# Kernel optimization log

Hardware: AMD Instinct MI355X
Metric: run time of the kernel (lower is better)

## Reference

```python
import jax, jax.numpy as jnp
import numpy as np

B, C, H, W = 8, 128, 64, 64

def setup_inputs() -> dict:
    key = jax.random.key(0)
    ks = jax.random.split(key, 8)
    s = 1.0 / np.sqrt(C)
    return {
        "x": jax.random.normal(ks[0], (B, C, H, W), dtype=jnp.float32),
        "dw_q": jax.random.normal(ks[1], (C,), dtype=jnp.float32) * s,
        "pw_q": jax.random.normal(ks[2], (C, C), dtype=jnp.float32) * s,
        "dw_k": jax.random.normal(ks[3], (C,), dtype=jnp.float32) * s,
        "pw_k": jax.random.normal(ks[4], (C, C), dtype=jnp.float32) * s,
        "dw_v": jax.random.normal(ks[5], (C,), dtype=jnp.float32) * s,
        "pw_v": jax.random.normal(ks[6], (C, C), dtype=jnp.float32) * s,
        "gamma": jnp.zeros((1,), dtype=jnp.float32) + 0.5,
    }

def _proj(x, dw, pw):
    # depthwise 1x1 (groups=C, no bias) == per-channel scale; then pointwise 1x1 conv (C_out=C)
    xs = x * dw[None, :, None, None]
    return jnp.einsum('oc,bchw->bohw', pw, xs)

def reference(x, dw_q, pw_q, dw_k, pw_k, dw_v, pw_v, gamma):
    b, c, h, w = x.shape
    n = h * w
    q = _proj(x, dw_q, pw_q).reshape(b, c, n)   # B,C,N
    k = _proj(x, dw_k, pw_k).reshape(b, c, n)
    v = _proj(x, dw_v, pw_v).reshape(b, c, n)
    # energy[b,n,m] = sum_c q[b,c,n] k[b,c,m]  (no scaling, as in source)
    energy = jnp.einsum('bcn,bcm->bnm', q, k)
    attn = jax.nn.softmax(energy, axis=-1)      # B,N,N
    # out[b,c,n] = sum_m v[b,c,m] attn[b,n,m]
    out = jnp.einsum('bcm,bnm->bcn', v, attn).reshape(b, c, h, w)
    return gamma[0] * out + x
```

## Files before the change

### kernel.cpp

```cpp
#include <hip/hip_runtime.h>
#include <hip/hip_bf16.h>


typedef __bf16 v8bf __attribute__((ext_vector_type(8)));
typedef float  v4f  __attribute__((ext_vector_type(4)));
typedef unsigned long long u64;

#define B_ 8
#define C_ 128
#define N_ 4096

#define SWZ(R, COLS) ((R) * 160 + (((((COLS) >> 3) ^ (((R) >> 2) & 15))) << 3) + ((COLS) & 7))

static __device__ __forceinline__ unsigned short f2bf_rne(float f) {
    union { float f; unsigned u; } v; v.f = f;
    return (unsigned short)((v.u + 0x7fffu + ((v.u >> 16) & 1u)) >> 16);
}

static __device__ __forceinline__ u64 bf8pack(uint4 s) {
    float f[8];
    #pragma unroll
    for (int j = 0; j < 8; ++j) {
        unsigned hs = (j & 1) ? ((&s.x)[j >> 1] >> 16) : ((&s.x)[j >> 1] & 0xffffu);
        union { unsigned u; float f; } t; t.u = hs << 16; f[j] = t.f;
    }
    int lo = __builtin_amdgcn_cvt_pk_fp8_f32(f[0], f[1], 0, false);
    lo     = __builtin_amdgcn_cvt_pk_fp8_f32(f[2], f[3], lo, true);
    int hi = __builtin_amdgcn_cvt_pk_fp8_f32(f[4], f[5], 0, false);
    hi     = __builtin_amdgcn_cvt_pk_fp8_f32(f[6], f[7], hi, true);
    return (u64)(unsigned)lo | ((u64)(unsigned)hi << 32);
}

__global__ __launch_bounds__(256, 2) void proj_kernel(
    const float* __restrict__ x,
    const float* __restrict__ dw_q, const float* __restrict__ pw_q,
    const float* __restrict__ dw_k, const float* __restrict__ pw_k,
    const float* __restrict__ dw_v, const float* __restrict__ pw_v,
    unsigned char* __restrict__ qf8, unsigned char* __restrict__ kt8,
    unsigned char* __restrict__ vt8)
{
    __shared__ unsigned short xT[128 * 160];
    __shared__ unsigned short Ws[128 * 160];

    const int bid = blockIdx.x;
    const int bb  = bid & 7;
    const int t   = (bid >> 3) & 31;
    const int pp  = bid >> 8;
    const int n0  = t * 128;
    const int tid = threadIdx.x;
    const int w    = tid >> 6;
    const int lane = tid & 63;
    const int quad = lane >> 4;
    const int l16  = lane & 15;

    #pragma unroll
    for (int k = 0; k < 16; ++k) {
        const int idx = tid + k * 256;
        const int c  = idx >> 5;
        const int nq = idx & 31;
        float4 f = *(const float4*)(x + ((size_t)(bb * C_ + c)) * N_ + n0 + nq * 4);
        xT[SWZ(nq * 4 + 0, c)] = f2bf_rne(f.x);
        xT[SWZ(nq * 4 + 1, c)] = f2bf_rne(f.y);
        xT[SWZ(nq * 4 + 2, c)] = f2bf_rne(f.z);
        xT[SWZ(nq * 4 + 3, c)] = f2bf_rne(f.w);
    }
    const float* pw = (pp == 0) ? pw_q : (pp == 1) ? pw_k : pw_v;
    const float* dw = (pp == 0) ? dw_q : (pp == 1) ? dw_k : dw_v;
    const float qs = (pp == 0) ? 1.4426950408889634f : 1.0f;
    #pragma unroll
    for (int k = 0; k < 16; ++k) {
        const int idx = tid + k * 256;
        const int o  = idx >> 5;
        const int c4 = (idx & 31) * 4;
        float4 p4 = *(const float4*)(pw + o * 128 + c4);
        float4 d4 = *(const float4*)(dw + c4);
        unsigned lo = (unsigned)f2bf_rne(p4.x * d4.x * qs) | ((unsigned)f2bf_rne(p4.y * d4.y * qs) << 16);
        unsigned hi = (unsigned)f2bf_rne(p4.z * d4.z * qs) | ((unsigned)f2bf_rne(p4.w * d4.w * qs) << 16);
        *(unsigned long long*)&Ws[SWZ(o, c4)] =
            (unsigned long long)lo | ((unsigned long long)hi << 32);
    }
    __syncthreads();

    const unsigned short* As = (pp < 2) ? xT : Ws;
    const unsigned short* Bs = (pp < 2) ? Ws : xT;

    v4f acc[2][8];
    #pragma unroll
    for (int i = 0; i < 2; ++i)
        #pragma unroll
        for (int j = 0; j < 8; ++j)
            acc[i][j] = (v4f){0.f, 0.f, 0.f, 0.f};

    #pragma unroll
    for (int kc = 0; kc < 4; ++kc) {
        v8bf av[2];
        #pragma unroll
        for (int i = 0; i < 2; ++i)
            av[i] = *(const v8bf*)&As[SWZ(w * 32 + i * 16 + l16, kc * 32 + quad * 8)];
        #pragma unroll
        for (int cb = 0; cb < 8; ++cb) {
            v8bf bv = *(const v8bf*)&Bs[SWZ(cb * 16 + l16, kc * 32 + quad * 8)];
            acc[0][cb] = __builtin_amdgcn_mfma_f32_16x16x32_bf16(av[0], bv, acc[0][cb], 0, 0, 0);
            acc[1][cb] = __builtin_amdgcn_mfma_f32_16x16x32_bf16(av[1], bv, acc[1][cb], 0, 0, 0);
        }
    }
    __syncthreads();

    unsigned short* sc = Ws;
    #pragma unroll
    for (int mi = 0; mi < 2; ++mi)
        #pragma unroll
        for (int cb = 0; cb < 8; ++cb)
            #pragma unroll
            for (int r = 0; r < 4; ++r)
                sc[SWZ(w * 32 + mi * 16 + quad * 4 + r, cb * 16 + l16)] =
                    f2bf_rne(acc[mi][cb][r]);
    __syncthreads();

    if (pp == 0) {
        unsigned char* dst = qf8 + (size_t)bb * 524288;
        #pragma unroll
        for (int p = 0; p < 8; ++p) {
            const int g     = p * 4 + w;
            const int strip = g >> 4, ni = (g >> 2) & 3, kc = g & 3;
            uint4 sv = *(const uint4*)&sc[SWZ(strip * 64 + ni * 16 + l16, kc * 32 + quad * 8)];
            *(u64*)(dst + (size_t)(t * 4 + strip * 2 + (ni >> 1)) * 4096
                        + ((ni & 1) * 2 + (kc >> 1)) * 1024 + lane * 16 + (kc & 1) * 8)
                = bf8pack(sv);
        }
    } else if (pp == 1) {
        unsigned char* dst = kt8 + (size_t)(bb * 32 + t) * 16384;
        #pragma unroll
        for (int p = 0; p < 8; ++p) {
            const int g  = p * 4 + w;
            const int mb = g >> 2, kc = g & 3;
            uint4 sv = *(const uint4*)&sc[SWZ(mb * 16 + l16, kc * 32 + quad * 8)];
            *(u64*)(dst + (mb * 2 + (kc >> 1)) * 1024 + lane * 16 + (kc & 1) * 8)
                = bf8pack(sv);
        }
    } else {
        unsigned char* dst = vt8 + (size_t)(bb * 32 + t) * 16384;
        #pragma unroll
        for (int p = 0; p < 8; ++p) {
            const int d   = p * 256 + tid;
            const int cb  = d >> 8;
            const int wqm = (d >> 6) & 3;
            const int q16 = (d >> 4) & 15;
            const int l   = d & 15;
            const int lnS = d & 63;
            uint4 sv = *(const uint4*)&sc[SWZ(cb * 16 + l, q16 * 8)];
            *(u64*)(dst + ((cb >> 1) * 4 + wqm) * 1024 + lnS * 16 + (cb & 1) * 8)
                = bf8pack(sv);
        }
    }
}

#define MFMA8(A, B, C) __builtin_amdgcn_mfma_f32_16x16x32_fp8_fp8((long)(A), (long)(B), C, 0, 0, 0)
#define EXP2(X) __builtin_amdgcn_exp2f(X)
#define PK8(E0, E1, E2, E3, W) { \
    W = __builtin_amdgcn_cvt_pk_fp8_f32(E0, E1, 0, false); \
    W = __builtin_amdgcn_cvt_pk_fp8_f32(E2, E3, W, true); \
}

#define SPLIT16(U4, LO, HI) { \
    LO = (u64)(U4).x | ((u64)(U4).y << 32); \
    HI = (u64)(U4).z | ((u64)(U4).w << 32); \
}

#define LOADK(KF, TILE) { \
    const unsigned char* kp_ = kbase + (size_t)(TILE) * 16384; \
    _Pragma("unroll") \
    for (int mi_ = 0; mi_ < 2; ++mi_) \
        _Pragma("unroll") \
        for (int kcp_ = 0; kcp_ < 2; ++kcp_) { \
            uint4 u_ = *(const uint4*)(kp_ + (mi_ * 2 + kcp_) * 1024); \
            SPLIT16(u_, KF[mi_][kcp_ * 2], KF[mi_][kcp_ * 2 + 1]) \
        } \
}

#define LOADV(TILE) { \
    const unsigned char* vp_ = vbase + (size_t)(TILE) * 16384; \
    _Pragma("unroll") \
    for (int cbp_ = 0; cbp_ < 4; ++cbp_) { \
        uint4 u_ = *(const uint4*)(vp_ + cbp_ * 4096); \
        SPLIT16(u_, vf[cbp_ * 2], vf[cbp_ * 2 + 1]) \
    } \
}

#define MKPF8(NI, PK0, PK1) { \
    int s_ = (quad < 2) ? PK0 : PK1; \
    u64 lo_ = (unsigned)__builtin_amdgcn_ds_bpermute(la, s_); \
    u64 hi_ = (unsigned)__builtin_amdgcn_ds_bpermute(lb, s_); \
    pf[NI] = lo_ | (hi_ << 32); \
}

#define SCOMP0(KF, SC) { \
    _Pragma("unroll") \
    for (int mi_ = 0; mi_ < 2; ++mi_) \
        _Pragma("unroll") \
        for (int ni_ = 0; ni_ < 2; ++ni_) { \
            v4f a_ = MFMA8(KF[mi_][0], qf[ni_][0], Z4v); \
            _Pragma("unroll") \
            for (int kc_ = 1; kc_ < 4; ++kc_) \
                a_ = MFMA8(KF[mi_][kc_], qf[ni_][kc_], a_); \
            SC[mi_][ni_] = a_; \
        } \
}

#define FUSED(SC_IN, KF, SC_OUT) { \
    float e0_, e1_, e2_, e3_; \
    int pk00_, pk10_, pk01_, pk11_; \
    SC_OUT[0][0] = MFMA8(KF[0][0], qf[0][0], Z4v); \
    SC_OUT[0][1] = MFMA8(KF[0][0], qf[1][0], Z4v); \
    e0_ = EXP2(SC_IN[0][0][0]); e1_ = EXP2(SC_IN[0][0][1]); \
    e2_ = EXP2(SC_IN[0][0][2]); e3_ = EXP2(SC_IN[0][0][3]); \
    SC_OUT[0][0] = MFMA8(KF[0][1], qf[0][1], SC_OUT[0][0]); \
    SC_OUT[0][1] = MFMA8(KF[0][1], qf[1][1], SC_OUT[0][1]); \
    lpart[0] += (e0_ + e1_) + (e2_ + e3_); \
    PK8(e0_, e1_, e2_, e3_, pk00_) \
    SC_OUT[0][0] = MFMA8(KF[0][2], qf[0][2], SC_OUT[0][0]); \
    SC_OUT[0][1] = MFMA8(KF[0][2], qf[1][2], SC_OUT[0][1]); \
    e0_ = EXP2(SC_IN[1][0][0]); e1_ = EXP2(SC_IN[1][0][1]); \
    e2_ = EXP2(SC_IN[1][0][2]); e3_ = EXP2(SC_IN[1][0][3]); \
    SC_OUT[0][0] = MFMA8(KF[0][3], qf[0][3], SC_OUT[0][0]); \
    SC_OUT[0][1] = MFMA8(KF[0][3], qf[1][3], SC_OUT[0][1]); \
    lpart[0] += (e0_ + e1_) + (e2_ + e3_); \
    PK8(e0_, e1_, e2_, e3_, pk10_) \
    SC_OUT[1][0] = MFMA8(KF[1][0], qf[0][0], Z4v); \
    SC_OUT[1][1] = MFMA8(KF[1][0], qf[1][0], Z4v); \
    MKPF8(0, pk00_, pk10_) \
    SC_OUT[1][0] = MFMA8(KF[1][1], qf[0][1], SC_OUT[1][0]); \
    SC_OUT[1][1] = MFMA8(KF[1][1], qf[1][1], SC_OUT[1][1]); \
    e0_ = EXP2(SC_IN[0][1][0]); e1_ = EXP2(SC_IN[0][1][1]); \
    e2_ = EXP2(SC_IN[0][1][2]); e3_ = EXP2(SC_IN[0][1][3]); \
    SC_OUT[1][0] = MFMA8(KF[1][2], qf[0][2], SC_OUT[1][0]); \
    SC_OUT[1][1] = MFMA8(KF[1][2], qf[1][2], SC_OUT[1][1]); \
    lpart[1] += (e0_ + e1_) + (e2_ + e3_); \
    PK8(e0_, e1_, e2_, e3_, pk01_) \
    SC_OUT[1][0] = MFMA8(KF[1][3], qf[0][3], SC_OUT[1][0]); \
    SC_OUT[1][1] = MFMA8(KF[1][3], qf[1][3], SC_OUT[1][1]); \
    e0_ = EXP2(SC_IN[1][1][0]); e1_ = EXP2(SC_IN[1][1][1]); \
    e2_ = EXP2(SC_IN[1][1][2]); e3_ = EXP2(SC_IN[1][1][3]); \
    lpart[1] += (e0_ + e1_) + (e2_ + e3_); \
    PK8(e0_, e1_, e2_, e3_, pk11_) \
    MKPF8(1, pk01_, pk11_) \
}

#define PVOP { \
    _Pragma("unroll") \
    for (int ni_ = 0; ni_ < 2; ++ni_) \
        _Pragma("unroll") \
        for (int cb_ = 0; cb_ < 8; ++cb_) \
            oacc[cb_][ni_] = MFMA8(vf[cb_], pf[ni_], oacc[cb_][ni_]); \
}

__global__ __launch_bounds__(256, 2) void attn_kernel(
    const unsigned char* __restrict__ qf8, const unsigned char* __restrict__ kt8,
    const unsigned char* __restrict__ vt8, const float* __restrict__ x,
    const float* __restrict__ gamma, float* __restrict__ out)
{
    __shared__ float red[32 * 132];
    __shared__ float l_s[4][32];

    const int bid = blockIdx.x;
    const int bb  = bid & 7;
    const int s   = bid >> 3;
    const int n0  = s * 32;
    const int tid = threadIdx.x;
    const int w    = tid >> 6;
    const int lane = tid & 63;
    const int quad = lane >> 4;
    const int l16  = lane & 15;

    u64 qf[2][4];
    {
        const unsigned char* qb = qf8 + (size_t)(bb * 128 + s) * 4096 + lane * 16;
        #pragma unroll
        for (int ni = 0; ni < 2; ++ni)
            #pragma unroll
            for (int kcp = 0; kcp < 2; ++kcp) {
                uint4 u = *(const uint4*)(qb + (ni * 2 + kcp) * 1024);
                SPLIT16(u, qf[ni][kcp * 2], qf[ni][kcp * 2 + 1])
            }
    }

    v4f oacc[8][2];
    #pragma unroll
    for (int i = 0; i < 8; ++i)
        #pragma unroll
        for (int j = 0; j < 2; ++j)
            oacc[i][j] = (v4f){0.f, 0.f, 0.f, 0.f};
    float lpart[2] = {0.f, 0.f};
    const v4f Z4v = {0.f, 0.f, 0.f, 0.f};

    const int la = ((((quad & 1) << 1) << 4) + l16) << 2;
    const int lb = la + 64;

    const unsigned char* kbase = kt8 + (size_t)(bb * 32) * 16384 + w * 4096 + lane * 16;
    const unsigned char* vbase = vt8 + (size_t)(bb * 32) * 16384 + w * 1024 + lane * 16;

    u64 kfA[2][4], kfB[2][4], vf[8], pf[2];
    v4f sc0[2][2], sc1[2][2];

    LOADK(kfA, 0)
    LOADV(0)
    LOADK(kfB, 1)
    SCOMP0(kfA, sc0)

    for (int it = 0; it < 32; it += 2) {
        LOADK(kfA, (it + 2) & 31)
        FUSED(sc0, kfB, sc1)
        PVOP
        LOADV((it + 1) & 31)
        LOADK(kfB, (it + 3) & 31)
        FUSED(sc1, kfA, sc0)
        PVOP
        LOADV((it + 2) & 31)
    }

    #pragma unroll
    for (int ni = 0; ni < 2; ++ni) {
        float r = lpart[ni];
        r += __shfl_xor(r, 16);
        r += __shfl_xor(r, 32);
        if (lane < 16) l_s[w][ni * 16 + lane] = r;
    }

    for (int rw = 0; rw < 4; ++rw) {
        if (w == rw) {
            #pragma unroll
            for (int cb = 0; cb < 8; ++cb)
                #pragma unroll
                for (int ni = 0; ni < 2; ++ni) {
                    float* p = &red[(ni * 16 + l16) * 132 + cb * 16 + quad * 4];
                    if (rw == 0) *(v4f*)p = oacc[cb][ni];
                    else {
                        v4f tv = *(const v4f*)p;
                        tv += oacc[cb][ni];
                        *(v4f*)p = tv;
                    }
                }
        }
        __syncthreads();
    }

    const float g = gamma[0];
    const int   n = tid & 31;
    const int  cg = tid >> 5;
    const float li = 1.0f / (((l_s[0][n] + l_s[1][n]) + (l_s[2][n] + l_s[3][n])));
    #pragma unroll
    for (int j = 0; j < 16; ++j) {
        const int c = cg * 16 + j;
        const size_t idx = ((size_t)(bb * C_ + c)) * N_ + n0 + n;
        out[idx] = g * red[n * 132 + c] * li + x[idx];
    }
}

extern "C" void kernel_launch(void* const* d_in, const int* in_sizes, int n_in,
                              void* d_out, int out_size, void* d_ws, size_t ws_size,
                              hipStream_t stream)
{
    (void)in_sizes; (void)n_in; (void)out_size; (void)ws_size;
    const float* x     = (const float*)d_in[0];
    const float* dw_q  = (const float*)d_in[1];
    const float* pw_q  = (const float*)d_in[2];
    const float* dw_k  = (const float*)d_in[3];
    const float* pw_k  = (const float*)d_in[4];
    const float* dw_v  = (const float*)d_in[5];
    const float* pw_v  = (const float*)d_in[6];
    const float* gamma = (const float*)d_in[7];
    float* out = (float*)d_out;

    unsigned char* qf8 = (unsigned char*)d_ws;
    unsigned char* kt8 = qf8 + (size_t)B_ * N_ * C_ / 2 * 2;
    unsigned char* vt8 = kt8 + (size_t)B_ * N_ * C_;

    proj_kernel<<<dim3(768), dim3(256), 0, stream>>>(
        x, dw_q, pw_q, dw_k, pw_k, dw_v, pw_v, qf8, kt8, vt8);
    attn_kernel<<<dim3(1024), dim3(256), 0, stream>>>(
        qf8, kt8, vt8, x, gamma, out);
}
```

Measured before the change: 154.1 us.

## Double-buffer V fragments and compute softmax row sums via MFMA with ones

V tile fragments are now held in two register buffers so each V load is issued a full iteration before its PV MFMA uses it, which gives the memory latency more time to hide. The softmax denominator is no longer summed with scalar adds and cross-lane shuffles. It is accumulated by an extra MFMA per row block that multiplies the packed fp8 probabilities by a constant all-ones fragment. This costs 16 more VGPRs for the second V buffer and two extra MFMAs per tile, and the row sums are now taken over the fp8-rounded probabilities. The workspace offset expression was also simplified without changing its value.

```diff
diff --git a/kernel.cpp b/kernel.cpp
--- a/kernel.cpp
+++ b/kernel.cpp
@@ -178,12 +178,12 @@
         } \
 }
 
-#define LOADV(TILE) { \
+#define LOADV(VF, TILE) { \
     const unsigned char* vp_ = vbase + (size_t)(TILE) * 16384; \
     _Pragma("unroll") \
     for (int cbp_ = 0; cbp_ < 4; ++cbp_) { \
         uint4 u_ = *(const uint4*)(vp_ + cbp_ * 4096); \
-        SPLIT16(u_, vf[cbp_ * 2], vf[cbp_ * 2 + 1]) \
+        SPLIT16(u_, VF[cbp_ * 2], VF[cbp_ * 2 + 1]) \
     } \
 }
 
@@ -216,7 +216,6 @@
     e2_ = EXP2(SC_IN[0][0][2]); e3_ = EXP2(SC_IN[0][0][3]); \
     SC_OUT[0][0] = MFMA8(KF[0][1], qf[0][1], SC_OUT[0][0]); \
     SC_OUT[0][1] = MFMA8(KF[0][1], qf[1][1], SC_OUT[0][1]); \
-    lpart[0] += (e0_ + e1_) + (e2_ + e3_); \
     PK8(e0_, e1_, e2_, e3_, pk00_) \
     SC_OUT[0][0] = MFMA8(KF[0][2], qf[0][2], SC_OUT[0][0]); \
     SC_OUT[0][1] = MFMA8(KF[0][2], qf[1][2], SC_OUT[0][1]); \
@@ -224,34 +223,33 @@
     e2_ = EXP2(SC_IN[1][0][2]); e3_ = EXP2(SC_IN[1][0][3]); \
     SC_OUT[0][0] = MFMA8(KF[0][3], qf[0][3], SC_OUT[0][0]); \
     SC_OUT[0][1] = MFMA8(KF[0][3], qf[1][3], SC_OUT[0][1]); \
-    lpart[0] += (e0_ + e1_) + (e2_ + e3_); \
     PK8(e0_, e1_, e2_, e3_, pk10_) \
     SC_OUT[1][0] = MFMA8(KF[1][0], qf[0][0], Z4v); \
     SC_OUT[1][1] = MFMA8(KF[1][0], qf[1][0], Z4v); \
     MKPF8(0, pk00_, pk10_) \
+    lacc[0] = MFMA8(ones8, pf[0], lacc[0]); \
     SC_OUT[1][0] = MFMA8(KF[1][1], qf[0][1], SC_OUT[1][0]); \
     SC_OUT[1][1] = MFMA8(KF[1][1], qf[1][1], SC_OUT[1][1]); \
     e0_ = EXP2(SC_IN[0][1][0]); e1_ = EXP2(SC_IN[0][1][1]); \
     e2_ = EXP2(SC_IN[0][1][2]); e3_ = EXP2(SC_IN[0][1][3]); \
     SC_OUT[1][0] = MFMA8(KF[1][2], qf[0][2], SC_OUT[1][0]); \
     SC_OUT[1][1] = MFMA8(KF[1][2], qf[1][2], SC_OUT[1][1]); \
-    lpart[1] += (e0_ + e1_) + (e2_ + e3_); \
     PK8(e0_, e1_, e2_, e3_, pk01_) \
     SC_OUT[1][0] = MFMA8(KF[1][3], qf[0][3], SC_OUT[1][0]); \
     SC_OUT[1][1] = MFMA8(KF[1][3], qf[1][3], SC_OUT[1][1]); \
     e0_ = EXP2(SC_IN[1][1][0]); e1_ = EXP2(SC_IN[1][1][1]); \
     e2_ = EXP2(SC_IN[1][1][2]); e3_ = EXP2(SC_IN[1][1][3]); \
-    lpart[1] += (e0_ + e1_) + (e2_ + e3_); \
     PK8(e0_, e1_, e2_, e3_, pk11_) \
     MKPF8(1, pk01_, pk11_) \
-}
-
-#define PVOP { \
+    lacc[1] = MFMA8(ones8, pf[1], lacc[1]); \
+}
+
+#define PVOP(VF) { \
     _Pragma("unroll") \
     for (int ni_ = 0; ni_ < 2; ++ni_) \
         _Pragma("unroll") \
         for (int cb_ = 0; cb_ < 8; ++cb_) \
-            oacc[cb_][ni_] = MFMA8(vf[cb_], pf[ni_], oacc[cb_][ni_]); \
+            oacc[cb_][ni_] = MFMA8(VF[cb_], pf[ni_], oacc[cb_][ni_]); \
 }
 
 __global__ __launch_bounds__(256, 2) void attn_kernel(
@@ -290,8 +288,9 @@
         #pragma unroll
         for (int j = 0; j < 2; ++j)
             oacc[i][j] = (v4f){0.f, 0.f, 0.f, 0.f};
-    float lpart[2] = {0.f, 0.f};
+    v4f lacc[2] = {(v4f){0.f, 0.f, 0.f, 0.f}, (v4f){0.f, 0.f, 0.f, 0.f}};
     const v4f Z4v = {0.f, 0.f, 0.f, 0.f};
+    const u64 ones8 = 0x3838383838383838ull;
 
     const int la = ((((quad & 1) << 1) << 4) + l16) << 2;
     const int lb = la + 64;
@@ -299,32 +298,29 @@
     const unsigned char* kbase = kt8 + (size_t)(bb * 32) * 16384 + w * 4096 + lane * 16;
     const unsigned char* vbase = vt8 + (size_t)(bb * 32) * 16384 + w * 1024 + lane * 16;
 
-    u64 kfA[2][4], kfB[2][4], vf[8], pf[2];
+    u64 kfA[2][4], kfB[2][4], vfA[8], vfB[8], pf[2];
     v4f sc0[2][2], sc1[2][2];
 
     LOADK(kfA, 0)
-    LOADV(0)
+    LOADV(vfA, 0)
     LOADK(kfB, 1)
+    LOADV(vfB, 1)
     SCOMP0(kfA, sc0)
 
     for (int it = 0; it < 32; it += 2) {
         LOADK(kfA, (it + 2) & 31)
         FUSED(sc0, kfB, sc1)
-        PVOP
-        LOADV((it + 1) & 31)
+        PVOP(vfA)
+        LOADV(vfA, (it + 2) & 31)
         LOADK(kfB, (it + 3) & 31)
         FUSED(sc1, kfA, sc0)
-        PVOP
-        LOADV((it + 2) & 31)
-    }
-
-    #pragma unroll
-    for (int ni = 0; ni < 2; ++ni) {
-        float r = lpart[ni];
-        r += __shfl_xor(r, 16);
-        r += __shfl_xor(r, 32);
-        if (lane < 16) l_s[w][ni * 16 + lane] = r;
-    }
+        PVOP(vfB)
+        LOADV(vfB, (it + 3) & 31)
+    }
+
+    #pragma unroll
+    for (int ni = 0; ni < 2; ++ni)
+        if (lane < 16) l_s[w][ni * 16 + lane] = lacc[ni][0];
 
     for (int rw = 0; rw < 4; ++rw) {
         if (w == rw) {
@@ -372,7 +368,7 @@
     float* out = (float*)d_out;
 
     unsigned char* qf8 = (unsigned char*)d_ws;
-    unsigned char* kt8 = qf8 + (size_t)B_ * N_ * C_ / 2 * 2;
+    unsigned char* kt8 = qf8 + (size_t)B_ * N_ * C_;
     unsigned char* vt8 = kt8 + (size_t)B_ * N_ * C_;
 
     proj_kernel<<<dim3(768), dim3(256), 0, stream>>>(
```

New measurement: 157.2 us. No clear change (+2.0%).
